# Optimization experiments

Hardware: AMD Instinct MI355X
Metric: run time of the kernel (lower is better)

Reference implementation:

```python
import math
import jax, jax.numpy as jnp
import numpy as np

B, N, D = 4, 2048, 512
H, DV, DO = 8, 64, 512


def setup_inputs() -> dict:
    key = jax.random.key(0)
    ks = jax.random.split(key, 8)
    def xavier(k, shape, fan_in, fan_out):
        a = math.sqrt(6.0 / (fan_in + fan_out))
        return jax.random.uniform(k, shape, jnp.float32, -a, a)
    return {
        "query": jax.random.normal(ks[0], (B, N, D), jnp.float32),
        "key": jax.random.normal(ks[1], (B, N, D), jnp.float32),
        "value": jax.random.normal(ks[2], (B, N, D), jnp.float32),
        "attn_mask": jax.random.randint(ks[3], (N, N), 0, 2, jnp.int32),
        "Wq": xavier(ks[4], (H, D, D), D, D),
        "Wk": xavier(ks[5], (H, D, D), D, D),
        "Wv": xavier(ks[6], (H, D, DV), D, DV),
        "Wo": xavier(ks[7], (H * DV, DO), H * DV, DO),
    }


def reference(query, key, value, attn_mask, Wq, Wk, Wv, Wo):
    b, n, d = query.shape
    h, dv = Wv.shape[0], Wv.shape[2]
    # per-head projections: [b, h, n, d] / [b, h, n, dv]
    Q = jnp.einsum('bnd,hde->bhne', query, Wq)
    K = jnp.einsum('bnd,hde->bhne', key, Wk)
    V = jnp.einsum('bnd,hdv->bhnv', value, Wv)
    # multiplicative mask (1: do not attend -> zeroed score), scaled by sqrt(d)
    keep = (1.0 - attn_mask.astype(jnp.float32))[None, None]  # [1,1,n,n]
    QK = jnp.einsum('bhne,bhme->bhnm', Q, K) * keep / math.sqrt(d)
    attn_weights = QK  # linear_attention=True: skip softmax
    QKV = jnp.einsum('bhnm,bhmv->bhnv', attn_weights, V)  # [b,h,n,dv]
    out = QKV.transpose(0, 2, 1, 3).reshape(b, n, h * dv) @ Wo  # [b,n,do]
    return (out, attn_weights)
```

## Files before the change

kernel.cpp:

```cpp
#include <hip/hip_runtime.h>
#include <hip/hip_bf16.h>

#define DEVFN __device__ __forceinline__

constexpr int Bb = 4, Nn = 2048, Dd = 512, Hh = 8, DVv = 64, DOo = 512;

typedef short short8 __attribute__((ext_vector_type(8)));
typedef float f32x4 __attribute__((ext_vector_type(4)));

typedef __attribute__((address_space(1))) void GV;
typedef __attribute__((address_space(3))) void LV;

DEVFN unsigned short f32_bf16(float f) {
  unsigned u = __builtin_bit_cast(unsigned, f);
  u += 0x7fffu + ((u >> 16) & 1u);
  return (unsigned short)(u >> 16);
}

DEVFN void barrier_raw() {
  asm volatile("" ::: "memory");
  __builtin_amdgcn_s_barrier();
  asm volatile("" ::: "memory");
}

template<int Nv> DEVFN void wait_vmcnt() {
  if constexpr (Nv == 0)      asm volatile("s_waitcnt vmcnt(0)"  ::: "memory");
  else if constexpr (Nv == 6) asm volatile("s_waitcnt vmcnt(6)"  ::: "memory");
  else if constexpr (Nv == 8) asm volatile("s_waitcnt vmcnt(8)"  ::: "memory");
  else static_assert(Nv == 0 || Nv == 6 || Nv == 8, "bad vmcnt");
}
DEVFN void wait_lgkm0() { asm volatile("s_waitcnt lgkmcnt(0)" ::: "memory"); }

template<int ROWBYTES, int TOTAL>
DEVFN void stage_tile(const char* g, int strideBytes, char* lds, int tid) {
#pragma unroll
  for (int off = 0; off < TOTAL; off += 4096) {
    int o   = off + tid * 16;
    int row = o / ROWBYTES;
    int blk = (o >> 4) & ((ROWBYTES >> 4) - 1);
    int sb  = blk ^ (row & 7);
    const char* src = g + (size_t)row * strideBytes + (sb << 4);
    __builtin_amdgcn_global_load_lds((GV*)src, (LV*)(lds + o), 16, 0, 0);
  }
}

template<int ROWBYTES>
DEVFN short8 frag_ld(const char* lds, int row, int kbyte) {
  int blk = kbyte >> 4;
  int sb  = blk ^ (row & 7);
  return *(const short8*)(lds + row * ROWBYTES + (sb << 4));
}

DEVFN f32x4 mfma16(short8 a, short8 b, f32x4 c) {
  return __builtin_amdgcn_mfma_f32_16x16x32_bf16(a, b, c, 0, 0, 0);
}


__global__ void cvt_f32_bf16_kernel(const float* __restrict__ in,
                                    unsigned short* __restrict__ out, int n4) {
  int i = blockIdx.x * blockDim.x + threadIdx.x;
  if (i < n4) {
    float4 v = ((const float4*)in)[i];
    ushort4 o;
    o.x = f32_bf16(v.x); o.y = f32_bf16(v.y);
    o.z = f32_bf16(v.z); o.w = f32_bf16(v.w);
    ((ushort4*)out)[i] = o;
  }
}

__global__ void mask_prep_kernel(const int* __restrict__ m,
                                 unsigned short* __restrict__ ms, int n4) {
  int i = blockIdx.x * blockDim.x + threadIdx.x;
  if (i < n4) {
    int4 v = ((const int4*)m)[i];
    ushort4 o;
    o.x = v.x ? 0 : 0x3f80; o.y = v.y ? 0 : 0x3f80;
    o.z = v.z ? 0 : 0x3f80; o.w = v.w ? 0 : 0x3f80;
    ((ushort4*)ms)[i] = o;
  }
}

__global__ void transpose_w_kernel(const float* __restrict__ in,
                                   unsigned short* __restrict__ out, int R, int C) {
  __shared__ float t[32][33];
  int g = blockIdx.z;
  int c0 = blockIdx.x * 32, r0 = blockIdx.y * 32;
  const float* ip = in + (size_t)g * R * C;
  unsigned short* op = out + (size_t)g * R * C;
#pragma unroll
  for (int i = threadIdx.y; i < 32; i += 8)
    t[i][threadIdx.x] = ip[(size_t)(r0 + i) * C + c0 + threadIdx.x];
  __syncthreads();
#pragma unroll
  for (int i = threadIdx.y; i < 32; i += 8)
    op[(size_t)(c0 + i) * R + r0 + threadIdx.x] = f32_bf16(t[threadIdx.x][i]);
}

__global__ void transpose_u16_kernel(const unsigned short* __restrict__ in,
                                     unsigned short* __restrict__ out, int R, int C) {
  __shared__ unsigned short t[32][33];
  int g = blockIdx.z;
  int c0 = blockIdx.x * 32, r0 = blockIdx.y * 32;
  const unsigned short* ip = in + (size_t)g * R * C;
  unsigned short* op = out + (size_t)g * R * C;
#pragma unroll
  for (int i = threadIdx.y; i < 32; i += 8)
    t[i][threadIdx.x] = ip[(size_t)(r0 + i) * C + c0 + threadIdx.x];
  __syncthreads();
#pragma unroll
  for (int i = threadIdx.y; i < 32; i += 8)
    op[(size_t)(c0 + i) * R + r0 + threadIdx.x] = t[threadIdx.x][i];
}


template<int NCG, bool OUTF32>
__global__ __launch_bounds__(256)
void gemm_nt_kernel(const unsigned short* __restrict__ A,
                    const unsigned short* __restrict__ BtAll,
                    void* __restrict__ Cb, int HeadsOut, int Ncols) {
  constexpr int BN = NCG * 32;
  constexpr int NL = 4 + BN / 32;
  __shared__ alignas(16) char As[2][16384];
  __shared__ alignas(16) char Bs[2][BN * 128];
  int tid = threadIdx.x, lane = tid & 63;
  int w = tid >> 6, wr = w >> 1, wc = w & 1;
  int tM = blockIdx.x, tN = blockIdx.y, h = blockIdx.z;
  const char* Ab  = (const char*)A + ((size_t)tM * 128) * 1024;
  const char* Btb = (const char*)BtAll + ((size_t)h * Ncols + tN * BN) * 1024;

  f32x4 acc[4][NCG] = {};

  stage_tile<128, 16384>(Ab, 1024, As[0], tid);
  stage_tile<128, BN * 128>(Btb, 1024, Bs[0], tid);
#pragma unroll
  for (int kk = 0; kk < 8; ++kk) {
    int cur = kk & 1;
    if (kk < 7) {
      stage_tile<128, 16384>(Ab + (kk + 1) * 128, 1024, As[cur ^ 1], tid);
      stage_tile<128, BN * 128>(Btb + (kk + 1) * 128, 1024, Bs[cur ^ 1], tid);
      wait_vmcnt<NL>();
    } else {
      wait_vmcnt<0>();
    }
    barrier_raw();
#pragma unroll
    for (int c = 0; c < 2; ++c) {
      short8 af[4], bf[NCG];
#pragma unroll
      for (int rg = 0; rg < 4; ++rg)
        af[rg] = frag_ld<128>(As[cur], wr * 64 + rg * 16 + (lane & 15),
                              c * 64 + (lane >> 4) * 16);
#pragma unroll
      for (int cg = 0; cg < NCG; ++cg)
        bf[cg] = frag_ld<128>(Bs[cur], wc * (NCG * 16) + cg * 16 + (lane & 15),
                              c * 64 + (lane >> 4) * 16);
#pragma unroll
      for (int rg = 0; rg < 4; ++rg)
#pragma unroll
        for (int cg = 0; cg < NCG; ++cg)
          acc[rg][cg] = mfma16(af[rg], bf[cg], acc[rg][cg]);
    }
    barrier_raw();
  }

#pragma unroll
  for (int rg = 0; rg < 4; ++rg)
#pragma unroll
    for (int cg = 0; cg < NCG; ++cg)
#pragma unroll
      for (int r = 0; r < 4; ++r) {
        int grow = tM * 128 + wr * 64 + rg * 16 + (lane >> 4) * 4 + r;
        int col  = tN * BN + wc * (NCG * 16) + cg * 16 + (lane & 15);
        size_t orow = ((size_t)(grow >> 11) * HeadsOut + h) * 2048 + (grow & 2047);
        if constexpr (OUTF32)
          ((float*)Cb)[orow * Ncols + col] = acc[rg][cg][r];
        else
          ((unsigned short*)Cb)[orow * Ncols + col] = f32_bf16(acc[rg][cg][r]);
      }
}


__global__ __launch_bounds__(256)
void qk_attn_kernel(const unsigned short* __restrict__ Qb,
                    const unsigned short* __restrict__ Kb,
                    const unsigned short* __restrict__ ms,
                    float* __restrict__ attn_out) {
  __shared__ alignas(16) char As[2][16384];
  __shared__ alignas(16) char Bs[2][16384];
  int tid = threadIdx.x, lane = tid & 63;
  int w = tid >> 6, wr = w >> 1, wc = w & 1;
  int fid = blockIdx.x;
  int orig = (fid & 7) * 1024 + (fid >> 3);
  int tM = orig & 15, tN = (orig >> 4) & 15, bh = orig >> 8;

  const char* Ab  = (const char*)Qb + ((size_t)bh * Nn + tM * 128) * 1024;
  const char* Btb = (const char*)Kb + ((size_t)bh * Nn + tN * 128) * 1024;
  const float scale = 0.044194173824159216f;

  f32x4 acc[4][4] = {};

  stage_tile<128, 16384>(Ab, 1024, As[0], tid);
  stage_tile<128, 16384>(Btb, 1024, Bs[0], tid);
#pragma unroll
  for (int kk = 0; kk < 8; ++kk) {
    int cur = kk & 1;
    if (kk < 7) {
      stage_tile<128, 16384>(Ab + (kk + 1) * 128, 1024, As[cur ^ 1], tid);
      stage_tile<128, 16384>(Btb + (kk + 1) * 128, 1024, Bs[cur ^ 1], tid);
      wait_vmcnt<8>();
    } else {
      wait_vmcnt<0>();
    }
    barrier_raw();
#pragma unroll
    for (int c = 0; c < 2; ++c) {
      short8 af[4], bf[4];
#pragma unroll
      for (int rg = 0; rg < 4; ++rg)
        af[rg] = frag_ld<128>(As[cur], wr * 64 + rg * 16 + (lane & 15),
                              c * 64 + (lane >> 4) * 16);
#pragma unroll
      for (int cg = 0; cg < 4; ++cg)
        bf[cg] = frag_ld<128>(Bs[cur], wc * 64 + cg * 16 + (lane & 15),
                              c * 64 + (lane >> 4) * 16);
#pragma unroll
      for (int rg = 0; rg < 4; ++rg)
#pragma unroll
        for (int cg = 0; cg < 4; ++cg)
          acc[rg][cg] = mfma16(af[rg], bf[cg], acc[rg][cg]);
    }
    barrier_raw();
  }

#pragma unroll
  for (int rg = 0; rg < 4; ++rg)
#pragma unroll
    for (int cg = 0; cg < 4; ++cg)
#pragma unroll
      for (int r = 0; r < 4; ++r) {
        int rowL = wr * 64 + rg * 16 + (lane >> 4) * 4 + r;
        int colL = wc * 64 + cg * 16 + (lane & 15);
        int qrow = tM * 128 + rowL, kcol = tN * 128 + colL;
        unsigned short kv = ms[(size_t)qrow * Nn + kcol];
        float keep = __builtin_bit_cast(float, (unsigned)kv << 16);
        attn_out[((size_t)bh * Nn + qrow) * Nn + kcol] =
            acc[rg][cg][r] * scale * keep;
      }
}


__global__ __launch_bounds__(256)
void pv_kernel(const float* __restrict__ attn,
               const unsigned short* __restrict__ VbT,
               unsigned short* __restrict__ QKV) {
  __shared__ alignas(16) char As[2][16384];
  __shared__ alignas(16) char Bs[2][8192];
  int tid = threadIdx.x, lane = tid & 63;
  int w = tid >> 6, wr = w >> 1, wc = w & 1;
  int tM = blockIdx.x, bh = blockIdx.y;
  int b = bh >> 3, h = bh & 7;

  int arow = tid >> 1, ahalf = tid & 1;
  const float* Ag = attn + ((size_t)bh * Nn + (size_t)tM * 128 + arow) * Nn
                    + ahalf * 32;
  const char* Btb = (const char*)VbT + (size_t)bh * DVv * Nn * 2;

  f32x4 acc[4][2] = {};

  {
    float4 ar[8];
#pragma unroll
    for (int i = 0; i < 8; ++i) ar[i] = ((const float4*)Ag)[i];
    stage_tile<128, 8192>(Btb, Nn * 2, Bs[0], tid);
    wait_vmcnt<0>();
#pragma unroll
    for (int j = 0; j < 4; ++j) {
      short8 s;
#pragma unroll
      for (int e = 0; e < 4; ++e) {
        s[e]     = (short)f32_bf16(ar[2 * j][e]);
        s[e + 4] = (short)f32_bf16(ar[2 * j + 1][e]);
      }
      int sb = (ahalf * 4 + j) ^ (arow & 7);
      *(short8*)(As[0] + arow * 128 + (sb << 4)) = s;
    }
    wait_lgkm0();
    barrier_raw();
  }

#pragma unroll 2
  for (int kk = 0; kk < 32; ++kk) {
    int cur = kk & 1;
    float4 ar[8];
    if (kk < 31) {
      const float* an = Ag + (kk + 1) * 64;
#pragma unroll
      for (int i = 0; i < 8; ++i) ar[i] = ((const float4*)an)[i];
      stage_tile<128, 8192>(Btb + (kk + 1) * 128, Nn * 2, Bs[cur ^ 1], tid);
    }
#pragma unroll
    for (int c = 0; c < 2; ++c) {
      short8 af[4], bf2[2];
#pragma unroll
      for (int rg = 0; rg < 4; ++rg)
        af[rg] = frag_ld<128>(As[cur], wr * 64 + rg * 16 + (lane & 15),
                              c * 64 + (lane >> 4) * 16);
#pragma unroll
      for (int cg = 0; cg < 2; ++cg)
        bf2[cg] = frag_ld<128>(Bs[cur], wc * 32 + cg * 16 + (lane & 15),
                               c * 64 + (lane >> 4) * 16);
#pragma unroll
      for (int rg = 0; rg < 4; ++rg)
#pragma unroll
        for (int cg = 0; cg < 2; ++cg)
          acc[rg][cg] = mfma16(af[rg], bf2[cg], acc[rg][cg]);
    }
    if (kk < 31) {
      wait_vmcnt<0>();
#pragma unroll
      for (int j = 0; j < 4; ++j) {
        short8 s;
#pragma unroll
        for (int e = 0; e < 4; ++e) {
          s[e]     = (short)f32_bf16(ar[2 * j][e]);
          s[e + 4] = (short)f32_bf16(ar[2 * j + 1][e]);
        }
        int sb = (ahalf * 4 + j) ^ (arow & 7);
        *(short8*)(As[cur ^ 1] + arow * 128 + (sb << 4)) = s;
      }
      wait_lgkm0();
    }
    barrier_raw();
  }

#pragma unroll
  for (int rg = 0; rg < 4; ++rg)
#pragma unroll
    for (int cg = 0; cg < 2; ++cg)
#pragma unroll
      for (int r = 0; r < 4; ++r) {
        int rowL = wr * 64 + rg * 16 + (lane >> 4) * 4 + r;
        int colL = wc * 32 + cg * 16 + (lane & 15);
        size_t grow = (size_t)tM * 128 + rowL;
        QKV[((size_t)b * Nn + grow) * (Hh * DVv) + h * DVv + colL] =
            f32_bf16(acc[rg][cg][r]);
      }
}


extern "C" void kernel_launch(void* const* d_in, const int* in_sizes, int n_in,
                              void* d_out, int out_size, void* d_ws, size_t ws_size,
                              hipStream_t stream) {
  const float* q    = (const float*)d_in[0];
  const float* k    = (const float*)d_in[1];
  const float* v    = (const float*)d_in[2];
  const int*   mask = (const int*)d_in[3];
  const float* Wq   = (const float*)d_in[4];
  const float* Wk   = (const float*)d_in[5];
  const float* Wv   = (const float*)d_in[6];
  const float* Wo   = (const float*)d_in[7];

  char* ws = (char*)d_ws;
  size_t off = 0;
  auto alloc = [&](size_t bytes) {
    char* p = ws + off;
    off += (bytes + 255) & ~(size_t)255;
    return p;
  };
  unsigned short* WqT  = (unsigned short*)alloc((size_t)Hh * Dd * Dd * 2);
  unsigned short* WkT  = (unsigned short*)alloc((size_t)Hh * Dd * Dd * 2);
  unsigned short* WvT  = (unsigned short*)alloc((size_t)Hh * DVv * Dd * 2);
  unsigned short* WoT  = (unsigned short*)alloc((size_t)DOo * Hh * DVv * 2);
  unsigned short* Xq   = (unsigned short*)alloc((size_t)Bb * Nn * Dd * 2);
  unsigned short* Xk   = (unsigned short*)alloc((size_t)Bb * Nn * Dd * 2);
  unsigned short* Xv   = (unsigned short*)alloc((size_t)Bb * Nn * Dd * 2);
  unsigned short* Qb   = (unsigned short*)alloc((size_t)Bb * Hh * Nn * Dd * 2);
  unsigned short* Kb   = (unsigned short*)alloc((size_t)Bb * Hh * Nn * Dd * 2);
  unsigned short* Vb   = (unsigned short*)alloc((size_t)Bb * Hh * Nn * DVv * 2);
  unsigned short* VbT  = (unsigned short*)alloc((size_t)Bb * Hh * DVv * Nn * 2);
  unsigned short* QKVb = (unsigned short*)alloc((size_t)Bb * Nn * Hh * DVv * 2);
  unsigned short* Ms   = (unsigned short*)alloc((size_t)Nn * Nn * 2);

  int n4 = Bb * Nn * Dd / 4;
  cvt_f32_bf16_kernel<<<dim3(n4 / 256), dim3(256), 0, stream>>>(q, Xq, n4);
  cvt_f32_bf16_kernel<<<dim3(n4 / 256), dim3(256), 0, stream>>>(k, Xk, n4);
  cvt_f32_bf16_kernel<<<dim3(n4 / 256), dim3(256), 0, stream>>>(v, Xv, n4);
  mask_prep_kernel<<<dim3(Nn * Nn / 4 / 256), dim3(256), 0, stream>>>(mask, Ms, Nn * Nn / 4);

  transpose_w_kernel<<<dim3(Dd / 32, Dd / 32, Hh), dim3(32, 8), 0, stream>>>(Wq, WqT, Dd, Dd);
  transpose_w_kernel<<<dim3(Dd / 32, Dd / 32, Hh), dim3(32, 8), 0, stream>>>(Wk, WkT, Dd, Dd);
  transpose_w_kernel<<<dim3(DVv / 32, Dd / 32, Hh), dim3(32, 8), 0, stream>>>(Wv, WvT, Dd, DVv);
  transpose_w_kernel<<<dim3(DOo / 32, (Hh * DVv) / 32, 1), dim3(32, 8), 0, stream>>>(Wo, WoT, Hh * DVv, DOo);

  gemm_nt_kernel<4, false><<<dim3(64, 4, Hh), dim3(256), 0, stream>>>(Xq, WqT, Qb, Hh, Dd);
  gemm_nt_kernel<4, false><<<dim3(64, 4, Hh), dim3(256), 0, stream>>>(Xk, WkT, Kb, Hh, Dd);
  gemm_nt_kernel<2, false><<<dim3(64, 1, Hh), dim3(256), 0, stream>>>(Xv, WvT, Vb, Hh, DVv);

  transpose_u16_kernel<<<dim3(DVv / 32, Nn / 32, Bb * Hh), dim3(32, 8), 0, stream>>>(Vb, VbT, Nn, DVv);

  float* outp  = (float*)d_out;
  float* attnp = outp + (size_t)Bb * Nn * DOo;

  qk_attn_kernel<<<dim3(16 * 16 * Bb * Hh), dim3(256), 0, stream>>>(Qb, Kb, Ms, attnp);
  pv_kernel<<<dim3(16, Bb * Hh), dim3(256), 0, stream>>>(attnp, VbT, QKVb);

  gemm_nt_kernel<4, true><<<dim3(64, 4, 1), dim3(256), 0, stream>>>(QKVb, WoT, outp, 1, DOo);

  (void)in_sizes; (void)n_in; (void)out_size; (void)ws_size;
}
```

Before: 603.0 us.

## Chunk QK and PV launches by batch so attn tile is reread from cache

Splits the QK-attention and PV kernels into four interleaved launches of eight batch-heads each. Each PV launch can then reread the fp32 attention slice (about 128MB) while it may still sit in the large last-level cache, instead of streaming it back from HBM. The PV tile also shrinks from 128 to 64 rows, doubling the PV grid to 256 blocks per chunk so the GPU stays busy. The cost is extra launch overhead, smaller grids per launch, and less reuse of V per block.

New measurement: 605.3 us. No clear change (+0.4%).

```diff
diff --git a/kernel.cpp b/kernel.cpp
--- a/kernel.cpp
+++ b/kernel.cpp
@@ -184,14 +184,14 @@
 void qk_attn_kernel(const unsigned short* __restrict__ Qb,
                     const unsigned short* __restrict__ Kb,
                     const unsigned short* __restrict__ ms,
-                    float* __restrict__ attn_out) {
+                    float* __restrict__ attn_out, int bh0) {
   __shared__ alignas(16) char As[2][16384];
   __shared__ alignas(16) char Bs[2][16384];
   int tid = threadIdx.x, lane = tid & 63;
   int w = tid >> 6, wr = w >> 1, wc = w & 1;
   int fid = blockIdx.x;
-  int orig = (fid & 7) * 1024 + (fid >> 3);
-  int tM = orig & 15, tN = (orig >> 4) & 15, bh = orig >> 8;
+  int orig = (fid & 7) * 256 + (fid >> 3);
+  int tM = orig & 15, tN = (orig >> 4) & 15, bh = bh0 + (orig >> 8);
 
   const char* Ab  = (const char*)Qb + ((size_t)bh * Nn + tM * 128) * 1024;
   const char* Btb = (const char*)Kb + ((size_t)bh * Nn + tN * 128) * 1024;
@@ -252,38 +252,42 @@
 __global__ __launch_bounds__(256)
 void pv_kernel(const float* __restrict__ attn,
                const unsigned short* __restrict__ VbT,
-               unsigned short* __restrict__ QKV) {
-  __shared__ alignas(16) char As[2][16384];
+               unsigned short* __restrict__ QKV, int bh0) {
+  __shared__ alignas(16) char As[2][8192];
   __shared__ alignas(16) char Bs[2][8192];
   int tid = threadIdx.x, lane = tid & 63;
   int w = tid >> 6, wr = w >> 1, wc = w & 1;
-  int tM = blockIdx.x, bh = blockIdx.y;
+  int tM = blockIdx.x, bh = bh0 + blockIdx.y;
   int b = bh >> 3, h = bh & 7;
 
-  int arow = tid >> 1, ahalf = tid & 1;
-  const float* Ag = attn + ((size_t)bh * Nn + (size_t)tM * 128 + arow) * Nn
-                    + ahalf * 32;
+  int arow = tid >> 2, aseg = tid & 3;
+  const float* Ag = attn + ((size_t)bh * Nn + (size_t)tM * 64 + arow) * Nn
+                    + aseg * 16;
   const char* Btb = (const char*)VbT + (size_t)bh * DVv * Nn * 2;
 
-  f32x4 acc[4][2] = {};
+  f32x4 acc[2][2] = {};
+
+  auto packA = [&](float4 ar[4], char* dst) {
+    short8 s0, s1;
+#pragma unroll
+    for (int e = 0; e < 4; ++e) {
+      s0[e]     = (short)f32_bf16(ar[0][e]);
+      s0[e + 4] = (short)f32_bf16(ar[1][e]);
+      s1[e]     = (short)f32_bf16(ar[2][e]);
+      s1[e + 4] = (short)f32_bf16(ar[3][e]);
+    }
+    int b0 = (aseg * 2) ^ (arow & 7), b1 = (aseg * 2 + 1) ^ (arow & 7);
+    *(short8*)(dst + arow * 128 + (b0 << 4)) = s0;
+    *(short8*)(dst + arow * 128 + (b1 << 4)) = s1;
+  };
 
   {
-    float4 ar[8];
-#pragma unroll
-    for (int i = 0; i < 8; ++i) ar[i] = ((const float4*)Ag)[i];
+    float4 ar[4];
+#pragma unroll
+    for (int i = 0; i < 4; ++i) ar[i] = ((const float4*)Ag)[i];
     stage_tile<128, 8192>(Btb, Nn * 2, Bs[0], tid);
     wait_vmcnt<0>();
-#pragma unroll
-    for (int j = 0; j < 4; ++j) {
-      short8 s;
-#pragma unroll
-      for (int e = 0; e < 4; ++e) {
-        s[e]     = (short)f32_bf16(ar[2 * j][e]);
-        s[e + 4] = (short)f32_bf16(ar[2 * j + 1][e]);
-      }
-      int sb = (ahalf * 4 + j) ^ (arow & 7);
-      *(short8*)(As[0] + arow * 128 + (sb << 4)) = s;
-    }
+    packA(ar, As[0]);
     wait_lgkm0();
     barrier_raw();
   }
@@ -291,57 +295,47 @@
 #pragma unroll 2
   for (int kk = 0; kk < 32; ++kk) {
     int cur = kk & 1;
-    float4 ar[8];
+    float4 ar[4];
     if (kk < 31) {
       const float* an = Ag + (kk + 1) * 64;
 #pragma unroll
-      for (int i = 0; i < 8; ++i) ar[i] = ((const float4*)an)[i];
+      for (int i = 0; i < 4; ++i) ar[i] = ((const float4*)an)[i];
       stage_tile<128, 8192>(Btb + (kk + 1) * 128, Nn * 2, Bs[cur ^ 1], tid);
     }
 #pragma unroll
     for (int c = 0; c < 2; ++c) {
-      short8 af[4], bf2[2];
-#pragma unroll
-      for (int rg = 0; rg < 4; ++rg)
-        af[rg] = frag_ld<128>(As[cur], wr * 64 + rg * 16 + (lane & 15),
+      short8 af[2], bf2[2];
+#pragma unroll
+      for (int rg = 0; rg < 2; ++rg)
+        af[rg] = frag_ld<128>(As[cur], wr * 32 + rg * 16 + (lane & 15),
                               c * 64 + (lane >> 4) * 16);
 #pragma unroll
       for (int cg = 0; cg < 2; ++cg)
         bf2[cg] = frag_ld<128>(Bs[cur], wc * 32 + cg * 16 + (lane & 15),
                                c * 64 + (lane >> 4) * 16);
 #pragma unroll
-      for (int rg = 0; rg < 4; ++rg)
+      for (int rg = 0; rg < 2; ++rg)
 #pragma unroll
         for (int cg = 0; cg < 2; ++cg)
           acc[rg][cg] = mfma16(af[rg], bf2[cg], acc[rg][cg]);
     }
     if (kk < 31) {
       wait_vmcnt<0>();
-#pragma unroll
-      for (int j = 0; j < 4; ++j) {
-        short8 s;
-#pragma unroll
-        for (int e = 0; e < 4; ++e) {
-          s[e]     = (short)f32_bf16(ar[2 * j][e]);
-          s[e + 4] = (short)f32_bf16(ar[2 * j + 1][e]);
-        }
-        int sb = (ahalf * 4 + j) ^ (arow & 7);
-        *(short8*)(As[cur ^ 1] + arow * 128 + (sb << 4)) = s;
-      }
+      packA(ar, As[cur ^ 1]);
       wait_lgkm0();
     }
     barrier_raw();
   }
 
 #pragma unroll
-  for (int rg = 0; rg < 4; ++rg)
+  for (int rg = 0; rg < 2; ++rg)
 #pragma unroll
     for (int cg = 0; cg < 2; ++cg)
 #pragma unroll
       for (int r = 0; r < 4; ++r) {
-        int rowL = wr * 64 + rg * 16 + (lane >> 4) * 4 + r;
+        int rowL = wr * 32 + rg * 16 + (lane >> 4) * 4 + r;
         int colL = wc * 32 + cg * 16 + (lane & 15);
-        size_t grow = (size_t)tM * 128 + rowL;
+        size_t grow = (size_t)tM * 64 + rowL;
         QKV[((size_t)b * Nn + grow) * (Hh * DVv) + h * DVv + colL] =
             f32_bf16(acc[rg][cg][r]);
       }
@@ -401,8 +395,10 @@
   float* outp  = (float*)d_out;
   float* attnp = outp + (size_t)Bb * Nn * DOo;
 
-  qk_attn_kernel<<<dim3(16 * 16 * Bb * Hh), dim3(256), 0, stream>>>(Qb, Kb, Ms, attnp);
-  pv_kernel<<<dim3(16, Bb * Hh), dim3(256), 0, stream>>>(attnp, VbT, QKVb);
+  for (int c = 0; c < 4; ++c) {
+    qk_attn_kernel<<<dim3(2048), dim3(256), 0, stream>>>(Qb, Kb, Ms, attnp, c * 8);
+    pv_kernel<<<dim3(32, 8), dim3(256), 0, stream>>>(attnp, VbT, QKVb, c * 8);
+  }
 
   gemm_nt_kernel<4, true><<<dim3(64, 4, 1), dim3(256), 0, stream>>>(QKVb, WoT, outp, 1, DOo);
 
```
